# Optimization experiments

Measured on AMD Instinct MI355X. Metric: run time of the kernel, lower is better.

Reference implementation:

```python
import jax, jax.numpy as jnp
import numpy as np

HIDDEN, LATENT, SYM, BOX = 512, 256, 64, 128
LEAF = 16384
NODE = 2 * LEAF - 1  # 32767: complete binary tree, leaves first
W_SCALE = 0.05  # keep tanh unsaturated


def setup_inputs() -> dict:
    key = jax.random.key(0)
    ks = jax.random.split(key, 16)
    # kids: valid tree structure (randint per-spec would give invalid child pointers).
    # Leaves are nodes [0, LEAF); internal node LEAF+j merges nodes 2j and 2j+1
    # (1-indexed pointers 2j+1, 2j+2). Every 4th internal node is a symmetry node.
    j = np.arange(NODE - LEAF)
    kids = np.zeros((1, NODE, 3), dtype=np.int32)
    kids[0, LEAF:, 0] = 2 * j + 1
    kids[0, LEAF:, 1] = 2 * j + 2
    kids[0, LEAF:, 2] = (j % 4 == 3).astype(np.int32)
    f32 = jnp.float32
    return {
        "kids": jnp.asarray(kids),
        "shape": jax.random.normal(ks[0], (1, BOX, LEAF), dtype=f32),
        "param": jax.random.normal(ks[1], (1, NODE, SYM), dtype=f32),
        # leaf / box encoder: box -> latent
        "Wb": jax.random.normal(ks[2], (BOX, LATENT), dtype=f32) * W_SCALE,
        "bb": jnp.zeros((LATENT,), dtype=f32),
        # adjacency encoder: (latent, latent) -> hidden -> latent
        "Wl": jax.random.normal(ks[3], (LATENT, HIDDEN), dtype=f32) * W_SCALE,
        "Wr": jax.random.normal(ks[4], (LATENT, HIDDEN), dtype=f32) * W_SCALE,
        "b1": jnp.zeros((HIDDEN,), dtype=f32),
        "W2": jax.random.normal(ks[5], (HIDDEN, LATENT), dtype=f32) * W_SCALE,
        "b2": jnp.zeros((LATENT,), dtype=f32),
        # symmetry encoder: (latent, sym) -> hidden -> latent
        "Wsl": jax.random.normal(ks[6], (LATENT, HIDDEN), dtype=f32) * W_SCALE,
        "Wsr": jax.random.normal(ks[7], (SYM, HIDDEN), dtype=f32) * W_SCALE,
        "bs1": jnp.zeros((HIDDEN,), dtype=f32),
        "Ws2": jax.random.normal(ks[8], (HIDDEN, LATENT), dtype=f32) * W_SCALE,
        "bs2": jnp.zeros((LATENT,), dtype=f32),
    }


def reference(kids, shape, param, Wb, bb, Wl, Wr, b1, W2, b2, Wsl, Wsr, bs1, Ws2, bs2):
    nodeNum = kids.shape[1]
    leafNum = shape.shape[2]
    latent = Wb.shape[1]

    # Leaves (nodes 0..leafNum-1, kids[...,0]==0) have no data dependence on hOut:
    # encode them all at once. boxes: [leafNum, box]
    boxes = jnp.transpose(shape[0])
    hLeaf = jnp.tanh(boxes @ Wb + bb)  # [leafNum, latent]
    hOut = jnp.zeros((nodeNum, latent), dtype=shape.dtype).at[:leafNum].set(hLeaf)

    p = param[0]  # [nodeNum, sym]
    k = kids[0]   # [nodeNum, 3]

    def step(h, x):
        i, k0, k1, k2 = x
        a = h[k0 - 1]      # [latent] left child hidden
        b = h[k1 - 1]      # [latent] right child hidden (adjacency case)
        s = p[k0 - 1]      # [sym]    (source indexes param with kids[...,0]-1)
        # adjacency merge
        h1 = jnp.tanh(jnp.tanh(a @ Wl + b @ Wr + b1) @ W2 + b2)
        # symmetry merge
        h2 = jnp.tanh(jnp.tanh(a @ Wsl + s @ Wsr + bs1) @ Ws2 + bs2)
        hi = jnp.where(k2 == 1, h2, h1)
        return h.at[i].set(hi), None

    # internal nodes are i in [leafNum, nodeNum); original only defines inputs there
    idx = jnp.arange(leafNum, nodeNum)
    xs = (idx, k[leafNum:, 0], k[leafNum:, 1], k[leafNum:, 2])
    hOut, _ = jax.lax.scan(step, hOut, xs)
    return hOut[nodeNum - 1][None, :]  # [1, latent], the root code
```

## Files before the change

kernel.cpp:

```cpp
#include <hip/hip_runtime.h>

#define LEAF   16384
#define NNODE  (2*LEAF-1)
#define LATENT 256
#define HIDDEN 512
#define SYM    64
#define BOX    128

using half8 = __attribute__((ext_vector_type(8))) _Float16;
using f32x4 = __attribute__((ext_vector_type(4))) float;

__device__ __forceinline__ f32x4 mfma16h(half8 a, half8 b, f32x4 c){
    return __builtin_amdgcn_mfma_f32_16x16x32_f16(a, b, c, 0, 0, 0);
}

__global__ void pack_kernel(const float* __restrict__ A, const float* __restrict__ B,
                            int Ksplit, int N, int KS, _Float16* __restrict__ pk, int total)
{
    int t = blockIdx.x*256 + threadIdx.x;
    if (t >= total) return;
    int j = t & 7, l = (t>>3)&63, tile = (t>>9)&3;
    int rest = t >> 11;
    int ks = rest % KS, cb = rest / KS;
    int k   = ks*32 + ((l>>4)*8) + j;
    int col = cb*64 + tile*16 + (l&15);
    float wv = (k < Ksplit) ? A[(size_t)k*N + col] : B[(size_t)(k-Ksplit)*N + col];
    pk[((size_t)(cb*KS + ks)*4 + tile)*512 + (size_t)l*8 + j] = (_Float16)wv;
}

__global__ __launch_bounds__(256) void leaf_kernel(
    const float* __restrict__ shape, const float* __restrict__ Wb,
    const float* __restrict__ bb, _Float16* __restrict__ hh)
{
    __shared__ float Xs[16][132];
    const int r0 = blockIdx.x * 16;
    const int t  = threadIdx.x;
    for (int it = 0; it < 2; ++it) {
        int task = t + it * 256;
        int r  = task & 15;
        int kg = task >> 4;
        #pragma unroll
        for (int j = 0; j < 4; ++j)
            Xs[r][4*kg + j] = shape[(size_t)(4*kg + j) * LEAF + r0 + r];
    }
    __syncthreads();
    float acc[16];
    #pragma unroll
    for (int r = 0; r < 16; ++r) acc[r] = 0.f;
    const int c = t;
    for (int k = 0; k < BOX; k += 4) {
        float w0 = Wb[(k+0)*LATENT + c];
        float w1 = Wb[(k+1)*LATENT + c];
        float w2 = Wb[(k+2)*LATENT + c];
        float w3 = Wb[(k+3)*LATENT + c];
        #pragma unroll
        for (int r = 0; r < 16; ++r) {
            float4 x = *reinterpret_cast<const float4*>(&Xs[r][k]);
            acc[r] = fmaf(x.x, w0, acc[r]);
            acc[r] = fmaf(x.y, w1, acc[r]);
            acc[r] = fmaf(x.z, w2, acc[r]);
            acc[r] = fmaf(x.w, w3, acc[r]);
        }
    }
    float bias = bb[c];
    #pragma unroll
    for (int r = 0; r < 16; ++r)
        hh[(size_t)(r0 + r) * LATENT + c] = (_Float16)tanhf(acc[r] + bias);
}

template<int NSUB>
__device__ __forceinline__ void k1_body(
    int rb, int cb, int start, int n,
    const _Float16* __restrict__ hh, const float* __restrict__ param,
    const _Float16* __restrict__ wcatpk, const _Float16* __restrict__ wscatpk,
    const float* __restrict__ b1, const float* __restrict__ bs1,
    _Float16* __restrict__ U, _Float16* __restrict__ V)
{
    __shared__ __align__(16) _Float16 ldsB1[2*2048];
    const int t = threadIdx.x, lane = t & 63, w = t >> 6;
    const bool isV = cb >= 8;
    const int cbl = isV ? cb - 8 : cb;
    const int KS  = isV ? 10 : 16;
    const _Float16* pk = (isV ? wscatpk : wcatpk) + (size_t)cbl * KS * 2048;
    const int row0  = rb * NSUB * 64;
    const int cbase = 2 * (start - LEAF);

    f32x4 acc[NSUB][4];
    #pragma unroll
    for (int s = 0; s < NSUB; ++s)
        #pragma unroll
        for (int c = 0; c < 4; ++c) acc[s][c] = (f32x4){0.f,0.f,0.f,0.f};

    *(half8*)(ldsB1 + t*8) = *(const half8*)(pk + (size_t)t*8);
    __syncthreads();

    for (int ks = 0; ks < KS; ++ks) {
        const bool hasNext = ks + 1 < KS;
        half8 stg;
        if (hasNext) stg = *(const half8*)(pk + (size_t)(ks+1)*2048 + (size_t)t*8);
        half8 A[NSUB];
        #pragma unroll
        for (int s = 0; s < NSUB; ++s) {
            int m = row0 + (s*4 + w)*16 + (lane & 15);
            if (m >= n) m = n - 1;
            if (!isV || ks < 8) {
                int node = cbase + 2*m + (ks >= 8 ? 1 : 0);
                A[s] = *(const half8*)(hh + (size_t)node*256 + (size_t)(ks & 7)*32 + ((lane >> 4)*8));
            } else {
                const float* pp = param + (size_t)(cbase + 2*m)*64 + (ks - 8)*32 + (lane >> 4)*8;
                float4 p0 = *(const float4*)pp;
                float4 p1 = *(const float4*)(pp + 4);
                A[s][0]=(_Float16)p0.x; A[s][1]=(_Float16)p0.y; A[s][2]=(_Float16)p0.z; A[s][3]=(_Float16)p0.w;
                A[s][4]=(_Float16)p1.x; A[s][5]=(_Float16)p1.y; A[s][6]=(_Float16)p1.z; A[s][7]=(_Float16)p1.w;
            }
        }
        const _Float16* lb = ldsB1 + (ks & 1)*2048;
        #pragma unroll
        for (int tile = 0; tile < 4; ++tile) {
            half8 Bh = *(const half8*)(lb + tile*512 + lane*8);
            #pragma unroll
            for (int s = 0; s < NSUB; ++s)
                acc[s][tile] = mfma16h(A[s], Bh, acc[s][tile]);
        }
        if (hasNext)
            *(half8*)(ldsB1 + ((ks+1) & 1)*2048 + t*8) = stg;
        __syncthreads();
    }

    const float* bias = isV ? bs1 : b1;
    _Float16* o = isV ? V : U;
    #pragma unroll
    for (int s = 0; s < NSUB; ++s) {
        #pragma unroll
        for (int tile = 0; tile < 4; ++tile) {
            int col = cbl*64 + tile*16 + (lane & 15);
            float bv = bias[col];
            #pragma unroll
            for (int r = 0; r < 4; ++r) {
                int m = row0 + (s*4 + w)*16 + (lane >> 4)*4 + r;
                if (m < n)
                    o[(size_t)m*512 + col] = (_Float16)tanhf(acc[s][tile][r] + bv);
            }
        }
    }
}

template<int NSUB>
__device__ __forceinline__ void k2_body(
    int rb, int cb, int start, int n,
    const _Float16* __restrict__ U, const _Float16* __restrict__ V,
    const int* __restrict__ kids,
    const _Float16* __restrict__ w2pk, const _Float16* __restrict__ ws2pk,
    const float* __restrict__ b2, const float* __restrict__ bs2,
    _Float16* __restrict__ hh)
{
    __shared__ __align__(16) _Float16 ldsB2[2*2048];
    const int t = threadIdx.x, lane = t & 63, w = t >> 6;
    const bool isSym = cb >= 4;
    const int cbl = isSym ? cb - 4 : cb;
    const _Float16* pk = (isSym ? ws2pk : w2pk) + (size_t)cbl * 16 * 2048;
    const _Float16* Asrc = isSym ? V : U;
    const int row0 = rb * NSUB * 64;

    f32x4 acc[NSUB][4];
    #pragma unroll
    for (int s = 0; s < NSUB; ++s)
        #pragma unroll
        for (int c = 0; c < 4; ++c) acc[s][c] = (f32x4){0.f,0.f,0.f,0.f};

    *(half8*)(ldsB2 + t*8) = *(const half8*)(pk + (size_t)t*8);
    __syncthreads();

    for (int ks = 0; ks < 16; ++ks) {
        const bool hasNext = ks + 1 < 16;
        half8 stg;
        if (hasNext) stg = *(const half8*)(pk + (size_t)(ks+1)*2048 + (size_t)t*8);
        half8 A[NSUB];
        #pragma unroll
        for (int s = 0; s < NSUB; ++s) {
            int m = row0 + (s*4 + w)*16 + (lane & 15);
            if (m >= n) m = n - 1;
            A[s] = *(const half8*)(Asrc + (size_t)m*512 + (size_t)ks*32 + ((lane >> 4)*8));
        }
        const _Float16* lb = ldsB2 + (ks & 1)*2048;
        #pragma unroll
        for (int tile = 0; tile < 4; ++tile) {
            half8 Bh = *(const half8*)(lb + tile*512 + lane*8);
            #pragma unroll
            for (int s = 0; s < NSUB; ++s)
                acc[s][tile] = mfma16h(A[s], Bh, acc[s][tile]);
        }
        if (hasNext)
            *(half8*)(ldsB2 + ((ks+1) & 1)*2048 + t*8) = stg;
        __syncthreads();
    }

    const float* bias = isSym ? bs2 : b2;
    const int want = isSym ? 1 : 0;
    #pragma unroll
    for (int s = 0; s < NSUB; ++s) {
        #pragma unroll
        for (int tile = 0; tile < 4; ++tile) {
            int col = cbl*64 + tile*16 + (lane & 15);
            float bv = bias[col];
            #pragma unroll
            for (int r = 0; r < 4; ++r) {
                int m = row0 + (s*4 + w)*16 + (lane >> 4)*4 + r;
                if (m < n && kids[3*(start + m) + 2] == want)
                    hh[(size_t)(start + m)*256 + col] = (_Float16)tanhf(acc[s][tile][r] + bv);
            }
        }
    }
}

template<int NSUB>
__global__ __launch_bounds__(256) void k1_kernel(
    const _Float16* __restrict__ hh, const float* __restrict__ param,
    const _Float16* __restrict__ wcatpk, const _Float16* __restrict__ wscatpk,
    const float* __restrict__ b1, const float* __restrict__ bs1,
    _Float16* __restrict__ U, _Float16* __restrict__ V, int start, int n)
{
    k1_body<NSUB>(blockIdx.x, blockIdx.y, start, n, hh, param, wcatpk, wscatpk, b1, bs1, U, V);
}

template<int NSUB>
__global__ __launch_bounds__(256) void k2_kernel(
    const _Float16* __restrict__ U, const _Float16* __restrict__ V,
    const int* __restrict__ kids,
    const _Float16* __restrict__ w2pk, const _Float16* __restrict__ ws2pk,
    const float* __restrict__ b2, const float* __restrict__ bs2,
    _Float16* __restrict__ hh, int start, int n)
{
    k2_body<NSUB>(blockIdx.x, blockIdx.y, start, n, U, V, kids, w2pk, ws2pk, b2, bs2, hh);
}

__device__ __forceinline__ void k1_tail(
    int rb, int cb, int start, int n,
    const _Float16* __restrict__ hh, const float* __restrict__ param,
    const _Float16* wlds,
    const float* __restrict__ b1, const float* __restrict__ bs1,
    _Float16* __restrict__ U, _Float16* __restrict__ V)
{
    const int t = threadIdx.x, lane = t & 63, w = t >> 6;
    const bool isV = cb >= 8;
    const int cbl = isV ? cb - 8 : cb;
    const int KS  = isV ? 10 : 16;
    const int row0  = rb * 64;
    const int cbase = 2 * (start - LEAF);

    f32x4 acc[4];
    #pragma unroll
    for (int c = 0; c < 4; ++c) acc[c] = (f32x4){0.f,0.f,0.f,0.f};

    int m = row0 + w*16 + (lane & 15);
    if (m >= n) m = n - 1;

    for (int ks = 0; ks < KS; ++ks) {
        half8 A;
        if (!isV || ks < 8) {
            int node = cbase + 2*m + (ks >= 8 ? 1 : 0);
            A = *(const half8*)(hh + (size_t)node*256 + (size_t)(ks & 7)*32 + ((lane >> 4)*8));
        } else {
            const float* pp = param + (size_t)(cbase + 2*m)*64 + (ks - 8)*32 + (lane >> 4)*8;
            float4 p0 = *(const float4*)pp;
            float4 p1 = *(const float4*)(pp + 4);
            A[0]=(_Float16)p0.x; A[1]=(_Float16)p0.y; A[2]=(_Float16)p0.z; A[3]=(_Float16)p0.w;
            A[4]=(_Float16)p1.x; A[5]=(_Float16)p1.y; A[6]=(_Float16)p1.z; A[7]=(_Float16)p1.w;
        }
        const _Float16* lb = wlds + ks*2048;
        #pragma unroll
        for (int tile = 0; tile < 4; ++tile) {
            half8 Bh = *(const half8*)(lb + tile*512 + lane*8);
            acc[tile] = mfma16h(A, Bh, acc[tile]);
        }
    }

    const float* bias = isV ? bs1 : b1;
    _Float16* o = isV ? V : U;
    #pragma unroll
    for (int tile = 0; tile < 4; ++tile) {
        int col = cbl*64 + tile*16 + (lane & 15);
        float bv = bias[col];
        #pragma unroll
        for (int r = 0; r < 4; ++r) {
            int mm = row0 + w*16 + (lane >> 4)*4 + r;
            if (mm < n)
                o[(size_t)mm*512 + col] = (_Float16)tanhf(acc[tile][r] + bv);
        }
    }
}

__device__ __forceinline__ void k2_tail(
    int rb, int cb, int start, int n,
    const _Float16* __restrict__ U, const _Float16* __restrict__ V,
    const int* __restrict__ kids,
    const _Float16* wlds,
    const float* __restrict__ b2, const float* __restrict__ bs2,
    _Float16* __restrict__ hh)
{
    const int t = threadIdx.x, lane = t & 63, w = t >> 6;
    const bool isSym = cb >= 4;
    const int cbl = isSym ? cb - 4 : cb;
    const _Float16* Asrc = isSym ? V : U;
    const int row0 = rb * 64;

    f32x4 acc[4];
    #pragma unroll
    for (int c = 0; c < 4; ++c) acc[c] = (f32x4){0.f,0.f,0.f,0.f};

    int m = row0 + w*16 + (lane & 15);
    if (m >= n) m = n - 1;

    for (int ks = 0; ks < 16; ++ks) {
        half8 A = *(const half8*)(Asrc + (size_t)m*512 + (size_t)ks*32 + ((lane >> 4)*8));
        const _Float16* lb = wlds + ks*2048;
        #pragma unroll
        for (int tile = 0; tile < 4; ++tile) {
            half8 Bh = *(const half8*)(lb + tile*512 + lane*8);
            acc[tile] = mfma16h(A, Bh, acc[tile]);
        }
    }

    const float* bias = isSym ? bs2 : b2;
    const int want = isSym ? 1 : 0;
    #pragma unroll
    for (int tile = 0; tile < 4; ++tile) {
        int col = cbl*64 + tile*16 + (lane & 15);
        float bv = bias[col];
        #pragma unroll
        for (int r = 0; r < 4; ++r) {
            int mm = row0 + w*16 + (lane >> 4)*4 + r;
            if (mm < n && kids[3*(start + mm) + 2] == want)
                hh[(size_t)(start + mm)*256 + col] = (_Float16)tanhf(acc[tile][r] + bv);
        }
    }
}

__device__ __forceinline__ void gbar(unsigned* bar, unsigned target)
{
    __syncthreads();
    if (threadIdx.x == 0) {
        __threadfence();
        __hip_atomic_fetch_add(bar, 1u, __ATOMIC_RELEASE, __HIP_MEMORY_SCOPE_AGENT);
        while (__hip_atomic_load(bar, __ATOMIC_ACQUIRE, __HIP_MEMORY_SCOPE_AGENT) < target)
            __builtin_amdgcn_s_sleep(2);
    }
    __syncthreads();
    __threadfence();
}

__global__ __launch_bounds__(256) void tail_kernel(
    _Float16* __restrict__ hh, const float* __restrict__ param,
    const _Float16* __restrict__ wcatpk, const _Float16* __restrict__ wscatpk,
    const float* __restrict__ b1, const float* __restrict__ bs1,
    _Float16* __restrict__ U, _Float16* __restrict__ V,
    const int* __restrict__ kids,
    const _Float16* __restrict__ w2pk, const _Float16* __restrict__ ws2pk,
    const float* __restrict__ b2, const float* __restrict__ bs2,
    unsigned* __restrict__ bar)
{
    __shared__ __align__(16) _Float16 wlds[16*2048];
    const int b = blockIdx.x;
    const int t = threadIdx.x;

    const _Float16* src;
    int nh;
    if (b < 8)       { src = wcatpk  + (size_t)b*16*2048;      nh = 16*2048/8; }
    else if (b < 16) { src = wscatpk + (size_t)(b-8)*10*2048;  nh = 10*2048/8; }
    else if (b < 20) { src = w2pk    + (size_t)(b-16)*16*2048; nh = 16*2048/8; }
    else             { src = ws2pk   + (size_t)(b-20)*16*2048; nh = 16*2048/8; }
    for (int i = t; i < nh; i += 256)
        *(half8*)(wlds + (size_t)i*8) = *(const half8*)(src + (size_t)i*8);
    __syncthreads();

    const unsigned G = gridDim.x;
    unsigned tgt = 0;
    int start = LEAF + 8192 + 4096 + 2048 + 1024 + 512;
    for (int n = 256; n >= 1; n >>= 1) {
        int rt = (n + 63) >> 6;
        if (b < 16) {
            for (int r = 0; r < rt; ++r)
                k1_tail(r, b, start, n, hh, param, wlds, b1, bs1, U, V);
        }
        tgt += G; gbar(bar, tgt);
        if (b >= 16) {
            for (int r = 0; r < rt; ++r)
                k2_tail(r, b - 16, start, n, U, V, kids, wlds, b2, bs2, hh);
        }
        if (n > 1) { tgt += G; gbar(bar, tgt); }
        start += n;
    }
}

__global__ void final_kernel(const _Float16* __restrict__ hh, float* __restrict__ out)
{
    int c = threadIdx.x;
    out[c] = (float)hh[(size_t)(NNODE - 1)*256 + c];
}

extern "C" void kernel_launch(void* const* d_in, const int* in_sizes, int n_in,
                              void* d_out, int out_size, void* d_ws, size_t ws_size,
                              hipStream_t stream) {
    const int*   kids  = (const int*)  d_in[0];
    const float* shape = (const float*)d_in[1];
    const float* param = (const float*)d_in[2];
    const float* Wb    = (const float*)d_in[3];
    const float* bb    = (const float*)d_in[4];
    const float* Wl    = (const float*)d_in[5];
    const float* Wr    = (const float*)d_in[6];
    const float* b1    = (const float*)d_in[7];
    const float* W2    = (const float*)d_in[8];
    const float* b2    = (const float*)d_in[9];
    const float* Wsl   = (const float*)d_in[10];
    const float* Wsr   = (const float*)d_in[11];
    const float* bs1   = (const float*)d_in[12];
    const float* Ws2   = (const float*)d_in[13];
    const float* bs2   = (const float*)d_in[14];
    float* out = (float*)d_out;

    char* ws = (char*)d_ws;
    _Float16* hh      = (_Float16*)(ws + 0);
    _Float16* U       = (_Float16*)(ws + 16777216);
    _Float16* V       = (_Float16*)(ws + 25165824);
    _Float16* wcatpk  = (_Float16*)(ws + 33554432);
    _Float16* wscatpk = (_Float16*)(ws + 34078720);
    _Float16* w2pk    = (_Float16*)(ws + 34406400);
    _Float16* ws2pk   = (_Float16*)(ws + 34668544);
    unsigned* bar     = (unsigned*)(ws + 34930688);

    hipMemsetAsync(bar, 0, 256, stream);

    pack_kernel<<<1024, 256, 0, stream>>>(Wl,  Wr,  256, 512, 16, wcatpk,  262144);
    pack_kernel<<< 640, 256, 0, stream>>>(Wsl, Wsr, 256, 512, 10, wscatpk, 163840);
    pack_kernel<<< 512, 256, 0, stream>>>(W2,  W2,  512, 256, 16, w2pk,    131072);
    pack_kernel<<< 512, 256, 0, stream>>>(Ws2, Ws2, 512, 256, 16, ws2pk,   131072);

    leaf_kernel<<<LEAF/16, 256, 0, stream>>>(shape, Wb, bb, hh);

    int start = LEAF;
    for (int n = 8192; n >= 512; n >>= 1) {
        if (n == 8192) {
            k1_kernel<2><<<dim3(n/128, 16), 256, 0, stream>>>(hh, param, wcatpk, wscatpk,
                                                              b1, bs1, U, V, start, n);
        } else {
            k1_kernel<1><<<dim3(n/64, 16), 256, 0, stream>>>(hh, param, wcatpk, wscatpk,
                                                             b1, bs1, U, V, start, n);
        }
        k2_kernel<1><<<dim3(n/64, 8), 256, 0, stream>>>(U, V, kids, w2pk, ws2pk,
                                                        b2, bs2, hh, start, n);
        start += n;
    }

    tail_kernel<<<24, 256, 0, stream>>>(hh, param, wcatpk, wscatpk, b1, bs1,
                                        U, V, kids, w2pk, ws2pk, b2, bs2, bar);

    final_kernel<<<1, 256, 0, stream>>>(hh, out);
}
```

Measured before the change: 414.1 us.

## Use MFMA for leaf encoding, widen tail grid, relax barrier, fuse final copy

The leaf encoder moves from scalar FP32 FMA to FP16 MFMA, using a newly packed Wb and 64 rows per block. The persistent tail kernel grows from 24 to 48 blocks, with two row-halves per column block sharing the work. The grid barrier now uses a relaxed spin plus a single acquire fence instead of full thread fences. The separate final copy kernel is folded into the tail kernel. Together these aim to cut leaf compute time, the serial tail latency and one launch, at the cost of FP16 leaf inputs and more blocks taking part in each barrier.

```diff
diff --git a/kernel.cpp b/kernel.cpp
--- a/kernel.cpp
+++ b/kernel.cpp
@@ -28,44 +28,48 @@
     pk[((size_t)(cb*KS + ks)*4 + tile)*512 + (size_t)l*8 + j] = (_Float16)wv;
 }
 
-__global__ __launch_bounds__(256) void leaf_kernel(
-    const float* __restrict__ shape, const float* __restrict__ Wb,
+__global__ __launch_bounds__(256) void leaf_mfma_kernel(
+    const float* __restrict__ shape, const _Float16* __restrict__ wbpk,
     const float* __restrict__ bb, _Float16* __restrict__ hh)
 {
-    __shared__ float Xs[16][132];
-    const int r0 = blockIdx.x * 16;
-    const int t  = threadIdx.x;
-    for (int it = 0; it < 2; ++it) {
-        int task = t + it * 256;
-        int r  = task & 15;
-        int kg = task >> 4;
-        #pragma unroll
-        for (int j = 0; j < 4; ++j)
-            Xs[r][4*kg + j] = shape[(size_t)(4*kg + j) * LEAF + r0 + r];
-    }
-    __syncthreads();
-    float acc[16];
-    #pragma unroll
-    for (int r = 0; r < 16; ++r) acc[r] = 0.f;
-    const int c = t;
-    for (int k = 0; k < BOX; k += 4) {
-        float w0 = Wb[(k+0)*LATENT + c];
-        float w1 = Wb[(k+1)*LATENT + c];
-        float w2 = Wb[(k+2)*LATENT + c];
-        float w3 = Wb[(k+3)*LATENT + c];
-        #pragma unroll
-        for (int r = 0; r < 16; ++r) {
-            float4 x = *reinterpret_cast<const float4*>(&Xs[r][k]);
-            acc[r] = fmaf(x.x, w0, acc[r]);
-            acc[r] = fmaf(x.y, w1, acc[r]);
-            acc[r] = fmaf(x.z, w2, acc[r]);
-            acc[r] = fmaf(x.w, w3, acc[r]);
-        }
-    }
-    float bias = bb[c];
-    #pragma unroll
-    for (int r = 0; r < 16; ++r)
-        hh[(size_t)(r0 + r) * LATENT + c] = (_Float16)tanhf(acc[r] + bias);
+    const int t = threadIdx.x, lane = t & 63, w = t >> 6;
+    const int r0 = blockIdx.x * 64;
+    const int m = r0 + w*16 + (lane & 15);
+
+    half8 A[4];
+    #pragma unroll
+    for (int ks = 0; ks < 4; ++ks) {
+        #pragma unroll
+        for (int e = 0; e < 8; ++e) {
+            int k = ks*32 + (lane >> 4)*8 + e;
+            A[ks][e] = (_Float16)shape[(size_t)k*LEAF + m];
+        }
+    }
+
+    for (int cb = 0; cb < 4; ++cb) {
+        f32x4 acc[4];
+        #pragma unroll
+        for (int c = 0; c < 4; ++c) acc[c] = (f32x4){0.f,0.f,0.f,0.f};
+        #pragma unroll
+        for (int ks = 0; ks < 4; ++ks) {
+            const _Float16* pb = wbpk + (size_t)((cb*4 + ks)*4)*512;
+            #pragma unroll
+            for (int tile = 0; tile < 4; ++tile) {
+                half8 B = *(const half8*)(pb + tile*512 + lane*8);
+                acc[tile] = mfma16h(A[ks], B, acc[tile]);
+            }
+        }
+        #pragma unroll
+        for (int tile = 0; tile < 4; ++tile) {
+            int col = cb*64 + tile*16 + (lane & 15);
+            float bv = bb[col];
+            #pragma unroll
+            for (int r = 0; r < 4; ++r) {
+                int row = r0 + w*16 + (lane >> 4)*4 + r;
+                hh[(size_t)row*256 + col] = (_Float16)tanhf(acc[tile][r] + bv);
+            }
+        }
+    }
 }
 
 template<int NSUB>
@@ -340,13 +344,12 @@
 {
     __syncthreads();
     if (threadIdx.x == 0) {
-        __threadfence();
         __hip_atomic_fetch_add(bar, 1u, __ATOMIC_RELEASE, __HIP_MEMORY_SCOPE_AGENT);
-        while (__hip_atomic_load(bar, __ATOMIC_ACQUIRE, __HIP_MEMORY_SCOPE_AGENT) < target)
-            __builtin_amdgcn_s_sleep(2);
+        while (__hip_atomic_load(bar, __ATOMIC_RELAXED, __HIP_MEMORY_SCOPE_AGENT) < target)
+            __builtin_amdgcn_s_sleep(4);
     }
     __syncthreads();
-    __threadfence();
+    __builtin_amdgcn_fence(__ATOMIC_ACQUIRE, "agent");
 }
 
 __global__ __launch_bounds__(256) void tail_kernel(
@@ -357,18 +360,25 @@
     const int* __restrict__ kids,
     const _Float16* __restrict__ w2pk, const _Float16* __restrict__ ws2pk,
     const float* __restrict__ b2, const float* __restrict__ bs2,
-    unsigned* __restrict__ bar)
+    unsigned* __restrict__ bar, float* __restrict__ out)
 {
     __shared__ __align__(16) _Float16 wlds[16*2048];
     const int b = blockIdx.x;
     const int t = threadIdx.x;
-
+    const bool isK1 = b < 32;
+    int cb, rh;
     const _Float16* src;
     int nh;
-    if (b < 8)       { src = wcatpk  + (size_t)b*16*2048;      nh = 16*2048/8; }
-    else if (b < 16) { src = wscatpk + (size_t)(b-8)*10*2048;  nh = 10*2048/8; }
-    else if (b < 20) { src = w2pk    + (size_t)(b-16)*16*2048; nh = 16*2048/8; }
-    else             { src = ws2pk   + (size_t)(b-20)*16*2048; nh = 16*2048/8; }
+    if (isK1) {
+        cb = b & 15; rh = b >> 4;
+        if (cb < 8) { src = wcatpk  + (size_t)cb*16*2048;     nh = 16*256; }
+        else        { src = wscatpk + (size_t)(cb-8)*10*2048; nh = 10*256; }
+    } else {
+        int i = b - 32; cb = i & 7; rh = i >> 3;
+        if (cb < 4) src = w2pk  + (size_t)cb*16*2048;
+        else        src = ws2pk + (size_t)(cb-4)*16*2048;
+        nh = 16*256;
+    }
     for (int i = t; i < nh; i += 256)
         *(half8*)(wlds + (size_t)i*8) = *(const half8*)(src + (size_t)i*8);
     __syncthreads();
@@ -378,24 +388,20 @@
     int start = LEAF + 8192 + 4096 + 2048 + 1024 + 512;
     for (int n = 256; n >= 1; n >>= 1) {
         int rt = (n + 63) >> 6;
-        if (b < 16) {
-            for (int r = 0; r < rt; ++r)
-                k1_tail(r, b, start, n, hh, param, wlds, b1, bs1, U, V);
+        if (isK1) {
+            for (int r = rh; r < rt; r += 2)
+                k1_tail(r, cb, start, n, hh, param, wlds, b1, bs1, U, V);
         }
         tgt += G; gbar(bar, tgt);
-        if (b >= 16) {
-            for (int r = 0; r < rt; ++r)
-                k2_tail(r, b - 16, start, n, U, V, kids, wlds, b2, bs2, hh);
-        }
-        if (n > 1) { tgt += G; gbar(bar, tgt); }
+        if (!isK1) {
+            for (int r = rh; r < rt; r += 2)
+                k2_tail(r, cb, start, n, U, V, kids, wlds, b2, bs2, hh);
+        }
+        tgt += G; gbar(bar, tgt);
         start += n;
     }
-}
-
-__global__ void final_kernel(const _Float16* __restrict__ hh, float* __restrict__ out)
-{
-    int c = threadIdx.x;
-    out[c] = (float)hh[(size_t)(NNODE - 1)*256 + c];
+    if (b == 0)
+        out[t] = (float)hh[(size_t)(NNODE - 1)*256 + t];
 }
 
 extern "C" void kernel_launch(void* const* d_in, const int* in_sizes, int n_in,
@@ -426,7 +432,8 @@
     _Float16* wscatpk = (_Float16*)(ws + 34078720);
     _Float16* w2pk    = (_Float16*)(ws + 34406400);
     _Float16* ws2pk   = (_Float16*)(ws + 34668544);
-    unsigned* bar     = (unsigned*)(ws + 34930688);
+    _Float16* wbpk    = (_Float16*)(ws + 34930688);
+    unsigned* bar     = (unsigned*)(ws + 34996224);
 
     hipMemsetAsync(bar, 0, 256, stream);
 
@@ -434,8 +441,9 @@
     pack_kernel<<< 640, 256, 0, stream>>>(Wsl, Wsr, 256, 512, 10, wscatpk, 163840);
     pack_kernel<<< 512, 256, 0, stream>>>(W2,  W2,  512, 256, 16, w2pk,    131072);
     pack_kernel<<< 512, 256, 0, stream>>>(Ws2, Ws2, 512, 256, 16, ws2pk,   131072);
-
-    leaf_kernel<<<LEAF/16, 256, 0, stream>>>(shape, Wb, bb, hh);
+    pack_kernel<<< 128, 256, 0, stream>>>(Wb,  Wb,  128, 256,  4, wbpk,     32768);
+
+    leaf_mfma_kernel<<<LEAF/64, 256, 0, stream>>>(shape, wbpk, bb, hh);
 
     int start = LEAF;
     for (int n = 8192; n >= 512; n >>= 1) {
@@ -451,8 +459,6 @@
         start += n;
     }
 
-    tail_kernel<<<24, 256, 0, stream>>>(hh, param, wcatpk, wscatpk, b1, bs1,
-                                        U, V, kids, w2pk, ws2pk, b2, bs2, bar);
-
-    final_kernel<<<1, 256, 0, stream>>>(hh, out);
-}
+    tail_kernel<<<48, 256, 0, stream>>>(hh, param, wcatpk, wscatpk, b1, bs1,
+                                        U, V, kids, w2pk, ws2pk, b2, bs2, bar, out);
+}
```

Result: faster. 361.0 us (-12.8%).
